# Performance work log

Hardware: AMD Instinct MI355X
Metric: run time of the kernel (lower is better)

The kernel has to match this reference:

```python
import jax, jax.numpy as jnp
import numpy as np

NUM_ITEMS = 100000
HIDDEN = 128
NNZ = 1600000


def setup_inputs() -> dict:
    key = jax.random.key(0)
    k1, k2, k3, k4, k5, k6 = jax.random.split(key, 6)
    item_embedding_table = jax.random.normal(k1, (NUM_ITEMS, HIDDEN), dtype=jnp.float32)
    adj_rows = jnp.sort(jax.random.randint(k2, (NNZ,), 0, NUM_ITEMS, dtype=jnp.int32))
    adj_cols = jax.random.randint(k3, (NNZ,), 0, NUM_ITEMS, dtype=jnp.int32)
    adj_vals = jax.random.uniform(k4, (NNZ,), dtype=jnp.float32)
    # nn.Linear default init (uniform in +-1/sqrt(fan_in)) approximated by scaled normal
    W_weight = jax.random.normal(k5, (HIDDEN, HIDDEN), dtype=jnp.float32) / np.sqrt(HIDDEN)
    W_bias = jax.random.normal(k6, (HIDDEN,), dtype=jnp.float32) * 0.01
    return {
        "item_embedding_table": item_embedding_table,
        "adj_rows": adj_rows,
        "adj_cols": adj_cols,
        "adj_vals": adj_vals,
        "W_weight": W_weight,
        "W_bias": W_bias,
    }


def reference(item_embedding_table, adj_rows, adj_cols, adj_vals, W_weight, W_bias):
    # support = W(x): x @ W^T + b   (nn.Linear convention: weight [out, in])
    support = jnp.einsum("nd,hd->nh", item_embedding_table, W_weight) + W_bias  # [N, H]
    # output = sparse_coo(adj) @ support, via gather + segment-sum scatter
    msgs = adj_vals[:, None] * support[adj_cols]  # [nnz, H]
    output = jax.ops.segment_sum(msgs, adj_rows, num_segments=NUM_ITEMS)  # [N, H]
    return output
```

## Files before the change

kernel.cpp:

```cpp
#include <hip/hip_runtime.h>
#include <hip/hip_fp16.h>

#define N_ITEMS 100000
#define HID 128
#define NNZ_T 1600000
#define GEMM_TILES 1563
#define GEMM_BLOCKS 781
#define RP_BLOCKS 391
#define SPMM_BLOCKS 25000

typedef unsigned short ushort_t;
typedef unsigned int uint_t;
typedef short bf16x8 __attribute__((ext_vector_type(8)));
typedef float f32x4 __attribute__((ext_vector_type(4)));

static __device__ __forceinline__ ushort_t f32_to_bf16(float f) {
    uint_t u = __float_as_uint(f);
    uint_t r = (u + 0x7FFFu + ((u >> 16) & 1u)) >> 16;
    return (ushort_t)r;
}

__global__ __launch_bounds__(256) void prep_gemm(
    const float* __restrict__ X, const float* __restrict__ W,
    const float* __restrict__ bias, const int* __restrict__ rows,
    ushort_t* __restrict__ S, int* __restrict__ row_ptr) {
    if (blockIdx.x >= GEMM_BLOCKS) {
        int r = (blockIdx.x - GEMM_BLOCKS) * 256 + threadIdx.x;
        if (r > N_ITEMS) return;
        int lo = 0, hi = NNZ_T;
        while (lo < hi) {
            int mid = (lo + hi) >> 1;
            if (rows[mid] < r) lo = mid + 1; else hi = mid;
        }
        row_ptr[r] = lo;
        return;
    }

    __shared__ ushort_t Wl[HID * HID];
    {
        const int t = threadIdx.x;
        const float4* Wf = (const float4*)W;
#pragma unroll
        for (int j = 0; j < 8; ++j) {
            const int gblk = j * 256 + t;
            float4 w0 = Wf[gblk * 2];
            float4 w1 = Wf[gblk * 2 + 1];
            bf16x8 v;
            v[0] = (short)f32_to_bf16(w0.x); v[1] = (short)f32_to_bf16(w0.y);
            v[2] = (short)f32_to_bf16(w0.z); v[3] = (short)f32_to_bf16(w0.w);
            v[4] = (short)f32_to_bf16(w1.x); v[5] = (short)f32_to_bf16(w1.y);
            v[6] = (short)f32_to_bf16(w1.z); v[7] = (short)f32_to_bf16(w1.w);
            const int ps = (gblk * 8) ^ (((gblk >> 4) & 7) << 3);
            *(bf16x8*)&Wl[ps] = v;
        }
    }
    __syncthreads();

    const int lane = threadIdx.x & 63;
    const int wave = threadIdx.x >> 6;
    const int m = lane & 15;
    const int q = lane >> 4;
    const int swz = (m & 7) << 3;

    for (int tile = blockIdx.x; tile < GEMM_TILES; tile += GEMM_BLOCKS) {
        const int row0 = tile * 64 + wave * 16;
        int arow = row0 + m;
        if (arow >= N_ITEMS) arow = N_ITEMS - 1;

        f32x4 acc[8] = {};
#pragma unroll
        for (int kb = 0; kb < 4; ++kb) {
            const int k0 = kb * 32 + q * 8;
            float4 a0 = *(const float4*)&X[(size_t)arow * HID + k0];
            float4 a1 = *(const float4*)&X[(size_t)arow * HID + k0 + 4];
            bf16x8 xf;
            xf[0] = (short)f32_to_bf16(a0.x); xf[1] = (short)f32_to_bf16(a0.y);
            xf[2] = (short)f32_to_bf16(a0.z); xf[3] = (short)f32_to_bf16(a0.w);
            xf[4] = (short)f32_to_bf16(a1.x); xf[5] = (short)f32_to_bf16(a1.y);
            xf[6] = (short)f32_to_bf16(a1.z); xf[7] = (short)f32_to_bf16(a1.w);
#pragma unroll
            for (int nt = 0; nt < 8; ++nt) {
                const bf16x8 wf = *(const bf16x8*)&Wl[((nt * 16 + m) * HID + k0) ^ swz];
                acc[nt] = __builtin_amdgcn_mfma_f32_16x16x32_bf16(wf, xf, acc[nt], 0, 0, 0);
            }
        }

        const int srow = row0 + m;
        const bool ok = srow < N_ITEMS;
#pragma unroll
        for (int nt = 0; nt < 8; ++nt) {
            const int c0 = nt * 16 + q * 4;
            float4 bv = *(const float4*)&bias[c0];
            ushort_t h0 = __half_as_ushort(__float2half(acc[nt][0] + bv.x));
            ushort_t h1 = __half_as_ushort(__float2half(acc[nt][1] + bv.y));
            ushort_t h2 = __half_as_ushort(__float2half(acc[nt][2] + bv.z));
            ushort_t h3 = __half_as_ushort(__float2half(acc[nt][3] + bv.w));
            uint2 pk;
            pk.x = (uint_t)h0 | ((uint_t)h1 << 16);
            pk.y = (uint_t)h2 | ((uint_t)h3 << 16);
            if (ok) *(uint2*)&S[(size_t)srow * HID + c0] = pk;
        }
    }
}

__global__ __launch_bounds__(256) void spmm_csr(
    const int* __restrict__ cols, const float* __restrict__ vals,
    const int* __restrict__ row_ptr, const ushort_t* __restrict__ S,
    float* __restrict__ out) {
    const int lane = threadIdx.x & 63;
    const int r = blockIdx.x * 4 + (threadIdx.x >> 6);
    if (r >= N_ITEMS) return;

    const int g = lane >> 4;
    const int l = lane & 15;

    int pa = row_ptr[r];
    const int pE = row_ptr[r + 1];

    __half2 acc[4];
#pragma unroll
    for (int j = 0; j < 4; ++j) acc[j] = __float2half2_rn(0.f);

    while (pa < pE) {
        const int idx  = pa + l;
        const int cidx = min(idx, pE - 1);
        const int c_l  = cols[cidx];
        const float v_l = (idx < pE) ? vals[cidx] : 0.f;

        uint4 u[4];
        float vv[4];
#pragma unroll
        for (int t = 0; t < 4; ++t) {
            const int s = 4 * t + g;
            const int ct = __shfl(c_l, s, 64);
            vv[t] = __shfl(v_l, s, 64);
            u[t] = *(const uint4*)&S[(size_t)ct * HID + 8 * l];
        }
#pragma unroll
        for (int t = 0; t < 4; ++t) {
            const __half2 w = __float2half2_rn(vv[t]);
            acc[0] = __hfma2(w, *(const __half2*)&u[t].x, acc[0]);
            acc[1] = __hfma2(w, *(const __half2*)&u[t].y, acc[1]);
            acc[2] = __hfma2(w, *(const __half2*)&u[t].z, acc[2]);
            acc[3] = __hfma2(w, *(const __half2*)&u[t].w, acc[3]);
        }
        pa += 16;
    }

    float f[8];
#pragma unroll
    for (int j = 0; j < 4; ++j) {
        f[2 * j] = __low2float(acc[j]);  f[2 * j + 1] = __high2float(acc[j]);
    }
#pragma unroll
    for (int e = 0; e < 8; ++e) {
        f[e] += __shfl_xor(f[e], 16, 64);
        f[e] += __shfl_xor(f[e], 32, 64);
    }
    if (g == 0) {
        float* p = &out[(size_t)r * HID + 8 * l];
        *(float4*)p       = make_float4(f[0], f[1], f[2], f[3]);
        *(float4*)(p + 4) = make_float4(f[4], f[5], f[6], f[7]);
    }
}

extern "C" void kernel_launch(void* const* d_in, const int* in_sizes, int n_in,
                              void* d_out, int out_size, void* d_ws, size_t ws_size,
                              hipStream_t stream) {
    const float* X    = (const float*)d_in[0];
    const int*   rows = (const int*)  d_in[1];
    const int*   cols = (const int*)  d_in[2];
    const float* vals = (const float*)d_in[3];
    const float* W    = (const float*)d_in[4];
    const float* bias = (const float*)d_in[5];
    float* out = (float*)d_out;

    ushort_t* S       = (ushort_t*)d_ws;
    int*      row_ptr = (int*)(S + (size_t)N_ITEMS * HID);

    prep_gemm<<<GEMM_BLOCKS + RP_BLOCKS, 256, 0, stream>>>(X, W, bias, rows, S, row_ptr);
    spmm_csr<<<SPMM_BLOCKS, 256, 0, stream>>>(cols, vals, row_ptr, S, out);
}
```

Before: 188.6 us.

## Split W bf16 conversion into prep kernel and read W from global in GEMM

Moves the fp32-to-bf16 conversion of W into a small separate prep kernel that also builds row_ptr. The GEMM becomes its own kernel with one 64-row tile per block and reads W fragments straight from global memory (L2-resident) instead of staging a swizzled copy in LDS. This drops the per-block LDS fill and barrier, but adds a kernel launch and replaces LDS reads with global/cache reads for every MFMA operand.

```diff
diff --git a/kernel.cpp b/kernel.cpp
--- a/kernel.cpp
+++ b/kernel.cpp
@@ -4,9 +4,9 @@
 #define N_ITEMS 100000
 #define HID 128
 #define NNZ_T 1600000
-#define GEMM_TILES 1563
-#define GEMM_BLOCKS 781
+#define PREPW_BLOCKS 64
 #define RP_BLOCKS 391
+#define GEMM_BLOCKS 1563
 #define SPMM_BLOCKS 25000
 
 typedef unsigned short ushort_t;
@@ -20,86 +20,67 @@
     return (ushort_t)r;
 }
 
-__global__ __launch_bounds__(256) void prep_gemm(
-    const float* __restrict__ X, const float* __restrict__ W,
-    const float* __restrict__ bias, const int* __restrict__ rows,
-    ushort_t* __restrict__ S, int* __restrict__ row_ptr) {
-    if (blockIdx.x >= GEMM_BLOCKS) {
-        int r = (blockIdx.x - GEMM_BLOCKS) * 256 + threadIdx.x;
-        if (r > N_ITEMS) return;
-        int lo = 0, hi = NNZ_T;
-        while (lo < hi) {
-            int mid = (lo + hi) >> 1;
-            if (rows[mid] < r) lo = mid + 1; else hi = mid;
-        }
-        row_ptr[r] = lo;
+__global__ void prep(const float* __restrict__ W, const int* __restrict__ rows,
+                     ushort_t* __restrict__ Wb, int* __restrict__ row_ptr) {
+    if (blockIdx.x < PREPW_BLOCKS) {
+        int i = blockIdx.x * 256 + threadIdx.x;
+        Wb[i] = f32_to_bf16(W[i]);
         return;
     }
+    int r = (blockIdx.x - PREPW_BLOCKS) * 256 + threadIdx.x;
+    if (r > N_ITEMS) return;
+    int lo = 0, hi = NNZ_T;
+    while (lo < hi) {
+        int mid = (lo + hi) >> 1;
+        if (rows[mid] < r) lo = mid + 1; else hi = mid;
+    }
+    row_ptr[r] = lo;
+}
 
-    __shared__ ushort_t Wl[HID * HID];
-    {
-        const int t = threadIdx.x;
-        const float4* Wf = (const float4*)W;
-#pragma unroll
-        for (int j = 0; j < 8; ++j) {
-            const int gblk = j * 256 + t;
-            float4 w0 = Wf[gblk * 2];
-            float4 w1 = Wf[gblk * 2 + 1];
-            bf16x8 v;
-            v[0] = (short)f32_to_bf16(w0.x); v[1] = (short)f32_to_bf16(w0.y);
-            v[2] = (short)f32_to_bf16(w0.z); v[3] = (short)f32_to_bf16(w0.w);
-            v[4] = (short)f32_to_bf16(w1.x); v[5] = (short)f32_to_bf16(w1.y);
-            v[6] = (short)f32_to_bf16(w1.z); v[7] = (short)f32_to_bf16(w1.w);
-            const int ps = (gblk * 8) ^ (((gblk >> 4) & 7) << 3);
-            *(bf16x8*)&Wl[ps] = v;
-        }
-    }
-    __syncthreads();
-
+__global__ __launch_bounds__(256) void gemm_mfma(
+    const float* __restrict__ X, const ushort_t* __restrict__ Wb,
+    const float* __restrict__ bias, ushort_t* __restrict__ S) {
     const int lane = threadIdx.x & 63;
     const int wave = threadIdx.x >> 6;
     const int m = lane & 15;
     const int q = lane >> 4;
-    const int swz = (m & 7) << 3;
+    const int row0 = blockIdx.x * 64 + wave * 16;
 
-    for (int tile = blockIdx.x; tile < GEMM_TILES; tile += GEMM_BLOCKS) {
-        const int row0 = tile * 64 + wave * 16;
-        int arow = row0 + m;
-        if (arow >= N_ITEMS) arow = N_ITEMS - 1;
+    int arow = row0 + m;
+    if (arow >= N_ITEMS) arow = N_ITEMS - 1;
 
-        f32x4 acc[8] = {};
+    f32x4 acc[8] = {};
 #pragma unroll
-        for (int kb = 0; kb < 4; ++kb) {
-            const int k0 = kb * 32 + q * 8;
-            float4 a0 = *(const float4*)&X[(size_t)arow * HID + k0];
-            float4 a1 = *(const float4*)&X[(size_t)arow * HID + k0 + 4];
-            bf16x8 xf;
-            xf[0] = (short)f32_to_bf16(a0.x); xf[1] = (short)f32_to_bf16(a0.y);
-            xf[2] = (short)f32_to_bf16(a0.z); xf[3] = (short)f32_to_bf16(a0.w);
-            xf[4] = (short)f32_to_bf16(a1.x); xf[5] = (short)f32_to_bf16(a1.y);
-            xf[6] = (short)f32_to_bf16(a1.z); xf[7] = (short)f32_to_bf16(a1.w);
-#pragma unroll
-            for (int nt = 0; nt < 8; ++nt) {
-                const bf16x8 wf = *(const bf16x8*)&Wl[((nt * 16 + m) * HID + k0) ^ swz];
-                acc[nt] = __builtin_amdgcn_mfma_f32_16x16x32_bf16(wf, xf, acc[nt], 0, 0, 0);
-            }
-        }
-
-        const int srow = row0 + m;
-        const bool ok = srow < N_ITEMS;
+    for (int kb = 0; kb < 4; ++kb) {
+        const int k0 = kb * 32 + q * 8;
+        float4 a0 = *(const float4*)&X[(size_t)arow * HID + k0];
+        float4 a1 = *(const float4*)&X[(size_t)arow * HID + k0 + 4];
+        bf16x8 xf;
+        xf[0] = (short)f32_to_bf16(a0.x); xf[1] = (short)f32_to_bf16(a0.y);
+        xf[2] = (short)f32_to_bf16(a0.z); xf[3] = (short)f32_to_bf16(a0.w);
+        xf[4] = (short)f32_to_bf16(a1.x); xf[5] = (short)f32_to_bf16(a1.y);
+        xf[6] = (short)f32_to_bf16(a1.z); xf[7] = (short)f32_to_bf16(a1.w);
 #pragma unroll
         for (int nt = 0; nt < 8; ++nt) {
-            const int c0 = nt * 16 + q * 4;
-            float4 bv = *(const float4*)&bias[c0];
-            ushort_t h0 = __half_as_ushort(__float2half(acc[nt][0] + bv.x));
-            ushort_t h1 = __half_as_ushort(__float2half(acc[nt][1] + bv.y));
-            ushort_t h2 = __half_as_ushort(__float2half(acc[nt][2] + bv.z));
-            ushort_t h3 = __half_as_ushort(__float2half(acc[nt][3] + bv.w));
-            uint2 pk;
-            pk.x = (uint_t)h0 | ((uint_t)h1 << 16);
-            pk.y = (uint_t)h2 | ((uint_t)h3 << 16);
-            if (ok) *(uint2*)&S[(size_t)srow * HID + c0] = pk;
+            const bf16x8 wf = *(const bf16x8*)&Wb[(size_t)(nt * 16 + m) * HID + k0];
+            acc[nt] = __builtin_amdgcn_mfma_f32_16x16x32_bf16(wf, xf, acc[nt], 0, 0, 0);
         }
+    }
+
+    const int srow = row0 + m;
+    const bool ok = srow < N_ITEMS;
+#pragma unroll
+    for (int nt = 0; nt < 8; ++nt) {
+        const int c0 = nt * 16 + q * 4;
+        float4 bv = *(const float4*)&bias[c0];
+        ushort_t h0 = __half_as_ushort(__float2half(acc[nt][0] + bv.x));
+        ushort_t h1 = __half_as_ushort(__float2half(acc[nt][1] + bv.y));
+        ushort_t h2 = __half_as_ushort(__float2half(acc[nt][2] + bv.z));
+        ushort_t h3 = __half_as_ushort(__float2half(acc[nt][3] + bv.w));
+        uint2 pk;
+        pk.x = (uint_t)h0 | ((uint_t)h1 << 16);
+        pk.y = (uint_t)h2 | ((uint_t)h3 << 16);
+        if (ok) *(uint2*)&S[(size_t)srow * HID + c0] = pk;
     }
 }
 
@@ -175,9 +156,11 @@
     const float* bias = (const float*)d_in[5];
     float* out = (float*)d_out;
 
-    ushort_t* S       = (ushort_t*)d_ws;
+    ushort_t* Wb      = (ushort_t*)d_ws;
+    ushort_t* S       = Wb + HID * HID;
     int*      row_ptr = (int*)(S + (size_t)N_ITEMS * HID);
 
-    prep_gemm<<<GEMM_BLOCKS + RP_BLOCKS, 256, 0, stream>>>(X, W, bias, rows, S, row_ptr);
+    prep<<<PREPW_BLOCKS + RP_BLOCKS, 256, 0, stream>>>(W, rows, Wb, row_ptr);
+    gemm_mfma<<<GEMM_BLOCKS, 256, 0, stream>>>(X, Wb, bias, S);
     spmm_csr<<<SPMM_BLOCKS, 256, 0, stream>>>(cols, vals, row_ptr, S, out);
 }
```

Result: slower. 206.2 us (+9.4%).

## Fuse GEMM and SpMM into one persistent cooperative kernel with grid sync

Applied to the files above, without the earlier changes.

Merges the row-pointer/GEMM prep kernel and the CSR SpMM kernel into a single cooperative kernel sized to device occupancy. Row-pointer search, GEMM tiles and SpMM rows are distributed with grid-stride loops, separated by a grid-wide barrier. This removes one kernel launch and the inter-kernel gap. It adds grid-sync cost, and persistent looping may reduce latency hiding compared to many independent blocks.

```diff
diff --git a/kernel.cpp b/kernel.cpp
--- a/kernel.cpp
+++ b/kernel.cpp
@@ -1,13 +1,14 @@
 #include <hip/hip_runtime.h>
 #include <hip/hip_fp16.h>
+#include <hip/hip_cooperative_groups.h>
+
+namespace cg = cooperative_groups;
 
 #define N_ITEMS 100000
 #define HID 128
 #define NNZ_T 1600000
 #define GEMM_TILES 1563
-#define GEMM_BLOCKS 781
-#define RP_BLOCKS 391
-#define SPMM_BLOCKS 25000
+#define MAX_BLOCKS 2048
 
 typedef unsigned short ushort_t;
 typedef unsigned int uint_t;
@@ -20,29 +21,32 @@
     return (ushort_t)r;
 }
 
-__global__ __launch_bounds__(256) void prep_gemm(
-    const float* __restrict__ X, const float* __restrict__ W,
-    const float* __restrict__ bias, const int* __restrict__ rows,
-    ushort_t* __restrict__ S, int* __restrict__ row_ptr) {
-    if (blockIdx.x >= GEMM_BLOCKS) {
-        int r = (blockIdx.x - GEMM_BLOCKS) * 256 + threadIdx.x;
-        if (r > N_ITEMS) return;
+__global__ __launch_bounds__(256) void gcn_fused(
+    const float* __restrict__ X, const int* __restrict__ rows,
+    const int* __restrict__ cols, const float* __restrict__ vals,
+    const float* __restrict__ W, const float* __restrict__ bias,
+    ushort_t* __restrict__ S, int* __restrict__ row_ptr,
+    float* __restrict__ out, int nblocks) {
+
+    const int tid = threadIdx.x;
+    const int lane = tid & 63;
+    const int wave = tid >> 6;
+
+    for (int r = blockIdx.x * 256 + tid; r <= N_ITEMS; r += nblocks * 256) {
         int lo = 0, hi = NNZ_T;
         while (lo < hi) {
             int mid = (lo + hi) >> 1;
             if (rows[mid] < r) lo = mid + 1; else hi = mid;
         }
         row_ptr[r] = lo;
-        return;
     }
 
     __shared__ ushort_t Wl[HID * HID];
     {
-        const int t = threadIdx.x;
         const float4* Wf = (const float4*)W;
 #pragma unroll
         for (int j = 0; j < 8; ++j) {
-            const int gblk = j * 256 + t;
+            const int gblk = j * 256 + tid;
             float4 w0 = Wf[gblk * 2];
             float4 w1 = Wf[gblk * 2 + 1];
             bf16x8 v;
@@ -56,13 +60,10 @@
     }
     __syncthreads();
 
-    const int lane = threadIdx.x & 63;
-    const int wave = threadIdx.x >> 6;
     const int m = lane & 15;
     const int q = lane >> 4;
     const int swz = (m & 7) << 3;
-
-    for (int tile = blockIdx.x; tile < GEMM_TILES; tile += GEMM_BLOCKS) {
+    for (int tile = blockIdx.x; tile < GEMM_TILES; tile += nblocks) {
         const int row0 = tile * 64 + wave * 16;
         int arow = row0 + m;
         if (arow >= N_ITEMS) arow = N_ITEMS - 1;
@@ -101,66 +102,61 @@
             if (ok) *(uint2*)&S[(size_t)srow * HID + c0] = pk;
         }
     }
-}
 
-__global__ __launch_bounds__(256) void spmm_csr(
-    const int* __restrict__ cols, const float* __restrict__ vals,
-    const int* __restrict__ row_ptr, const ushort_t* __restrict__ S,
-    float* __restrict__ out) {
-    const int lane = threadIdx.x & 63;
-    const int r = blockIdx.x * 4 + (threadIdx.x >> 6);
-    if (r >= N_ITEMS) return;
+    cg::this_grid().sync();
 
     const int g = lane >> 4;
     const int l = lane & 15;
 
-    int pa = row_ptr[r];
-    const int pE = row_ptr[r + 1];
+    for (int r = blockIdx.x * 4 + wave; r < N_ITEMS; r += nblocks * 4) {
+        int pa = row_ptr[r];
+        const int pE = row_ptr[r + 1];
 
-    __half2 acc[4];
+        __half2 acc[4];
 #pragma unroll
-    for (int j = 0; j < 4; ++j) acc[j] = __float2half2_rn(0.f);
+        for (int j = 0; j < 4; ++j) acc[j] = __float2half2_rn(0.f);
 
-    while (pa < pE) {
-        const int idx  = pa + l;
-        const int cidx = min(idx, pE - 1);
-        const int c_l  = cols[cidx];
-        const float v_l = (idx < pE) ? vals[cidx] : 0.f;
+        while (pa < pE) {
+            const int idx  = pa + l;
+            const int cidx = min(idx, pE - 1);
+            const int c_l  = cols[cidx];
+            const float v_l = (idx < pE) ? vals[cidx] : 0.f;
 
-        uint4 u[4];
-        float vv[4];
+            uint4 u[4];
+            float vv[4];
 #pragma unroll
-        for (int t = 0; t < 4; ++t) {
-            const int s = 4 * t + g;
-            const int ct = __shfl(c_l, s, 64);
-            vv[t] = __shfl(v_l, s, 64);
-            u[t] = *(const uint4*)&S[(size_t)ct * HID + 8 * l];
+            for (int t = 0; t < 4; ++t) {
+                const int s = 4 * t + g;
+                const int ct = __shfl(c_l, s, 64);
+                vv[t] = __shfl(v_l, s, 64);
+                u[t] = *(const uint4*)&S[(size_t)ct * HID + 8 * l];
+            }
+#pragma unroll
+            for (int t = 0; t < 4; ++t) {
+                const __half2 w = __float2half2_rn(vv[t]);
+                acc[0] = __hfma2(w, *(const __half2*)&u[t].x, acc[0]);
+                acc[1] = __hfma2(w, *(const __half2*)&u[t].y, acc[1]);
+                acc[2] = __hfma2(w, *(const __half2*)&u[t].z, acc[2]);
+                acc[3] = __hfma2(w, *(const __half2*)&u[t].w, acc[3]);
+            }
+            pa += 16;
+        }
+
+        float f[8];
+#pragma unroll
+        for (int j = 0; j < 4; ++j) {
+            f[2 * j] = __low2float(acc[j]);  f[2 * j + 1] = __high2float(acc[j]);
         }
 #pragma unroll
-        for (int t = 0; t < 4; ++t) {
-            const __half2 w = __float2half2_rn(vv[t]);
-            acc[0] = __hfma2(w, *(const __half2*)&u[t].x, acc[0]);
-            acc[1] = __hfma2(w, *(const __half2*)&u[t].y, acc[1]);
-            acc[2] = __hfma2(w, *(const __half2*)&u[t].z, acc[2]);
-            acc[3] = __hfma2(w, *(const __half2*)&u[t].w, acc[3]);
+        for (int e = 0; e < 8; ++e) {
+            f[e] += __shfl_xor(f[e], 16, 64);
+            f[e] += __shfl_xor(f[e], 32, 64);
         }
-        pa += 16;
-    }
-
-    float f[8];
-#pragma unroll
-    for (int j = 0; j < 4; ++j) {
-        f[2 * j] = __low2float(acc[j]);  f[2 * j + 1] = __high2float(acc[j]);
-    }
-#pragma unroll
-    for (int e = 0; e < 8; ++e) {
-        f[e] += __shfl_xor(f[e], 16, 64);
-        f[e] += __shfl_xor(f[e], 32, 64);
-    }
-    if (g == 0) {
-        float* p = &out[(size_t)r * HID + 8 * l];
-        *(float4*)p       = make_float4(f[0], f[1], f[2], f[3]);
-        *(float4*)(p + 4) = make_float4(f[4], f[5], f[6], f[7]);
+        if (g == 0) {
+            float* p = &out[(size_t)r * HID + 8 * l];
+            *(float4*)p       = make_float4(f[0], f[1], f[2], f[3]);
+            *(float4*)(p + 4) = make_float4(f[4], f[5], f[6], f[7]);
+        }
     }
 }
 
@@ -178,6 +174,23 @@
     ushort_t* S       = (ushort_t*)d_ws;
     int*      row_ptr = (int*)(S + (size_t)N_ITEMS * HID);
 
-    prep_gemm<<<GEMM_BLOCKS + RP_BLOCKS, 256, 0, stream>>>(X, W, bias, rows, S, row_ptr);
-    spmm_csr<<<SPMM_BLOCKS, 256, 0, stream>>>(cols, vals, row_ptr, S, out);
+    static int nblocks = 0;
+    if (nblocks == 0) {
+        int per_cu = 0;
+        hipOccupancyMaxActiveBlocksPerMultiprocessor(
+            &per_cu, reinterpret_cast<const void*>(gcn_fused), 256, 0);
+        int num_cu = 256;
+        hipDeviceProp_t prop;
+        if (hipGetDeviceProperties(&prop, 0) == hipSuccess && prop.multiProcessorCount > 0)
+            num_cu = prop.multiProcessorCount;
+        nblocks = (per_cu > 0 ? per_cu : 1) * num_cu;
+        if (nblocks > MAX_BLOCKS) nblocks = MAX_BLOCKS;
+        if (nblocks < 256) nblocks = 256;
+    }
+
+    void* args[] = {(void*)&X, (void*)&rows, (void*)&cols, (void*)&vals,
+                    (void*)&W, (void*)&bias, (void*)&S, (void*)&row_ptr,
+                    (void*)&out, (void*)&nblocks};
+    hipLaunchCooperativeKernel(reinterpret_cast<void*>(gcn_fused),
+                               dim3(nblocks), dim3(256), args, 0, stream);
 }
```

After: 342.5 us. 81.7% more time.
